# Optimization experiments

Hardware: AMD Instinct MI355X
Metric: run time of the kernel (lower is better)

## Reference

```python
import jax, jax.numpy as jnp
import numpy as np

NEG_MASK = -10000.0

def _sanitize(x):
    # torch.nan_to_num(x, nan=0.0, posinf=1.0, neginf=-1.0)
    return jnp.nan_to_num(x, nan=0.0, posinf=1.0, neginf=-1.0)

def setup_inputs() -> dict:
    key = jax.random.key(0)
    ks = jax.random.split(key, 7)
    Na, Nb, d = 4096, 4096, 256
    h = 4
    a_z = jax.random.normal(ks[0], (Na, d), dtype=jnp.float32)
    bv_z = jax.random.normal(ks[1], (Nb, d), dtype=jnp.float32)
    mask = jax.random.randint(ks[2], (Na, Nb), 0, 2) == 1
    weight = jax.random.normal(ks[3], (Na, Nb), dtype=jnp.float32)
    Wq = jax.random.normal(ks[4], (d, d), dtype=jnp.float32) * (1.0 / np.sqrt(d))
    Wk = jax.random.normal(ks[5], (d, d), dtype=jnp.float32) * (1.0 / np.sqrt(d))
    Wv = jax.random.normal(ks[6], (d, d), dtype=jnp.float32) * (1.0 / np.sqrt(d))
    return {"a_z": a_z, "bv_z": bv_z, "mask": mask, "weight": weight,
            "Wq": Wq, "Wk": Wk, "Wv": Wv, "h": h}

def reference(a_z, bv_z, mask, weight, Wq, Wk, Wv, h):
    d = a_z.shape[-1]
    dk = d // h
    # nan/inf sanitization (unconditional; identity on finite inputs, matching torch path)
    a_z = _sanitize(a_z)
    bv_z = _sanitize(bv_z)
    # projections; nn.Linear: x @ W.T. Reshape to [N, h, dk]
    q = (a_z @ Wq.T).reshape(-1, h, dk)   # [Na, h, dk]
    k = (bv_z @ Wk.T).reshape(-1, h, dk)  # [Nb, h, dk]
    v = (bv_z @ Wv.T).reshape(-1, h, dk)  # [Nb, h, dk]
    # attention scores [Na, h, Nb]
    att = jnp.einsum('ahd,bhd->ahb', q, k) / np.float32(np.sqrt(dk))
    att = jnp.where(mask[:, None, :], att, NEG_MASK)
    w = _sanitize(weight)
    att = att + w[:, None, :]
    att = jnp.clip(att, -10.0, 10.0)
    p = jax.nn.softmax(att, axis=-1)  # stable softmax (max-subtract) as in original
    # context: [Na, h, dk]; topic_align mean over heads -> [Na, dk]
    context = jnp.einsum('ahb,bhd->ahd', p, v)
    topic_align = context.mean(axis=1)
    influence = _sanitize(p.mean(axis=1).sum(axis=-1))  # [Na]
    return (topic_align, influence)
```

## Files before the change

### kernel.cpp

```cpp
#include <hip/hip_runtime.h>

#define NA 4096
#define NB 4096
#define DIM 256
#define DK 64
#define PSTR 72
#define WSTR 68
#define NSPLIT 8
#define BIT (NB / NSPLIT / 64)

typedef __attribute__((ext_vector_type(8))) short bf16x8;
typedef __attribute__((ext_vector_type(4))) float f32x4;
typedef __attribute__((ext_vector_type(4))) unsigned short us4;
typedef __attribute__((ext_vector_type(4))) int i32x4;

static __device__ __forceinline__ float bf2f(unsigned short u) {
    union { unsigned int u; float f; } x;
    x.u = ((unsigned int)u) << 16;
    return x.f;
}
static __device__ __forceinline__ unsigned short f2bf(float f) {
    union { float f; unsigned int u; } x;
    x.f = f;
    unsigned int r = x.u + 0x7fffu + ((x.u >> 16) & 1u);
    return (unsigned short)(r >> 16);
}


__global__ __launch_bounds__(256) void prep_kernel(
    const float* __restrict__ a_z, const float* __restrict__ bv,
    const float* __restrict__ Wq, const float* __restrict__ Wk,
    const float* __restrict__ Wv,
    unsigned short* __restrict__ ah, unsigned short* __restrict__ al,
    unsigned short* __restrict__ bh, unsigned short* __restrict__ bl,
    unsigned short* __restrict__ wh, unsigned short* __restrict__ wl)
{
    const int idx = blockIdx.x * 256 + threadIdx.x;
    const int y = blockIdx.y;
    const float* __restrict__ src;
    unsigned short* __restrict__ dh;
    unsigned short* __restrict__ dl;
    int row, col;
    if (y == 0) {
        src = a_z; dh = ah; dl = al;
        row = (idx >> 9) * 16 + (idx & 15);
        col = ((idx >> 6) & 7) * 32 + ((idx >> 4) & 3) * 8;
    } else if (y == 1) {
        src = bv; dh = bh; dl = bl;
        row = (idx >> 9) * 16 + (idx & 15);
        col = ((idx >> 6) & 7) * 32 + ((idx >> 4) & 3) * 8;
    } else {
        if (idx >= 3 * 8192) return;
        const int m = idx >> 13;
        const int im = idx & 8191;
        src = (m == 0) ? Wq : ((m == 1) ? Wk : Wv);
        dh = wh; dl = wl;
        row = (im >> 9) * 16 + (im & 15);
        col = ((im >> 6) & 7) * 32 + ((im >> 4) & 3) * 8;
    }
    f32x4 v0 = *(const f32x4*)(src + row * DIM + col);
    f32x4 v1 = *(const f32x4*)(src + row * DIM + col + 4);
    bf16x8 h8, l8;
    #pragma unroll
    for (int r = 0; r < 4; ++r) {
        unsigned short h0 = f2bf(v0[r]);
        h8[r] = (short)h0;  l8[r] = (short)f2bf(v0[r] - bf2f(h0));
        unsigned short h1 = f2bf(v1[r]);
        h8[4 + r] = (short)h1;  l8[4 + r] = (short)f2bf(v1[r] - bf2f(h1));
    }
    *(bf16x8*)(dh + idx * 8) = h8;
    *(bf16x8*)(dl + idx * 8) = l8;
}

__global__ __launch_bounds__(256, 2) void proj_kernel(
    const unsigned short* __restrict__ ah, const unsigned short* __restrict__ al,
    const unsigned short* __restrict__ bh, const unsigned short* __restrict__ bl,
    const unsigned short* __restrict__ whc, const unsigned short* __restrict__ wlc,
    unsigned short* __restrict__ qhi, unsigned short* __restrict__ qlo,
    unsigned short* __restrict__ khi, unsigned short* __restrict__ vtout)
{
    const int mat = blockIdx.z;
    const unsigned short* __restrict__ Xh = (mat == 0) ? ah : bh;
    const unsigned short* __restrict__ Xl = (mat == 0) ? al : bl;
    const unsigned short* __restrict__ Wh = whc + mat * 65536;
    const unsigned short* __restrict__ Wl = wlc + mat * 65536;

    const int tid  = threadIdx.x;
    const int wv   = tid >> 6;
    const int lane = tid & 63;
    const int c    = lane & 15;
    const int quad = lane >> 4;
    const int n0 = blockIdx.x * 64;
    const int by = blockIdx.y;

    const unsigned short* xhp = Xh + (n0 >> 4) * 4096 + lane * 8;
    const unsigned short* xlp = Xl + (n0 >> 4) * 4096 + lane * 8;
    const unsigned short* whp = Wh + (by * 4 + wv) * 4096 + lane * 8;
    const unsigned short* wlp = Wl + (by * 4 + wv) * 4096 + lane * 8;

    f32x4 acc[4];
    #pragma unroll
    for (int nt = 0; nt < 4; ++nt) acc[nt] = (f32x4){0.f, 0.f, 0.f, 0.f};

    bf16x8 wAh, wAl, xAh[4], xAl[4];
    bf16x8 wBh, wBl, xBh[4], xBl[4];

    wAh = *(const bf16x8*)(whp);
    wAl = *(const bf16x8*)(wlp);
    #pragma unroll
    for (int nt = 0; nt < 4; ++nt) {
        xAh[nt] = *(const bf16x8*)(xhp + nt * 4096);
        xAl[nt] = *(const bf16x8*)(xlp + nt * 4096);
    }

    #pragma unroll
    for (int kk = 0; kk < 8; kk += 2) {
        wBh = *(const bf16x8*)(whp + (kk + 1) * 512);
        wBl = *(const bf16x8*)(wlp + (kk + 1) * 512);
        #pragma unroll
        for (int nt = 0; nt < 4; ++nt) {
            xBh[nt] = *(const bf16x8*)(xhp + nt * 4096 + (kk + 1) * 512);
            xBl[nt] = *(const bf16x8*)(xlp + nt * 4096 + (kk + 1) * 512);
        }
        #pragma unroll
        for (int nt = 0; nt < 4; ++nt) {
            acc[nt] = __builtin_amdgcn_mfma_f32_16x16x32_bf16(xAh[nt], wAh, acc[nt], 0, 0, 0);
            acc[nt] = __builtin_amdgcn_mfma_f32_16x16x32_bf16(xAl[nt], wAh, acc[nt], 0, 0, 0);
            acc[nt] = __builtin_amdgcn_mfma_f32_16x16x32_bf16(xAh[nt], wAl, acc[nt], 0, 0, 0);
        }
        if (kk + 2 < 8) {
            wAh = *(const bf16x8*)(whp + (kk + 2) * 512);
            wAl = *(const bf16x8*)(wlp + (kk + 2) * 512);
            #pragma unroll
            for (int nt = 0; nt < 4; ++nt) {
                xAh[nt] = *(const bf16x8*)(xhp + nt * 4096 + (kk + 2) * 512);
                xAl[nt] = *(const bf16x8*)(xlp + nt * 4096 + (kk + 2) * 512);
            }
        }
        #pragma unroll
        for (int nt = 0; nt < 4; ++nt) {
            acc[nt] = __builtin_amdgcn_mfma_f32_16x16x32_bf16(xBh[nt], wBh, acc[nt], 0, 0, 0);
            acc[nt] = __builtin_amdgcn_mfma_f32_16x16x32_bf16(xBl[nt], wBh, acc[nt], 0, 0, 0);
            acc[nt] = __builtin_amdgcn_mfma_f32_16x16x32_bf16(xBh[nt], wBl, acc[nt], 0, 0, 0);
        }
    }

    if (mat != 2) {
        const int ks = wv >> 1;
        const int lq = ((wv & 1) * 2 + (c >> 3)) * 16 + quad * 4;
        const int e  = c & 7;
        #pragma unroll
        for (int nt = 0; nt < 4; ++nt) {
            const int tbase = (((by * 256 + (n0 >> 4) + nt) * 2 + ks) * 64 + lq) * 8 + e;
            #pragma unroll
            for (int r = 0; r < 4; ++r) {
                const int idx = tbase + r * 8;
                if (mat == 0) {
                    unsigned short h = f2bf(acc[nt][r]);
                    qhi[idx] = h;
                    qlo[idx] = f2bf(acc[nt][r] - bf2f(h));
                } else {
                    khi[idx] = f2bf(acc[nt][r]);
                }
            }
        }
    } else {
        #pragma unroll
        for (int nt = 0; nt < 4; ++nt) {
            const int lv = ((nt & 1) * 2 + (quad >> 1)) * 16 + c;
            const int idx = ((((by * 64 + (n0 >> 6)) * 4 + wv) * 2 + (nt >> 1)) * 64 + lv) * 8
                            + (quad & 1) * 4;
            us4 p;
            #pragma unroll
            for (int r = 0; r < 4; ++r) p[r] = f2bf(acc[nt][r]);
            *(us4*)(vtout + idx) = p;
        }
    }
}

__global__ __launch_bounds__(256, 2) void attn_kernel(
    const unsigned short* __restrict__ qhg,
    const unsigned short* __restrict__ qlg,
    const unsigned short* __restrict__ kg,
    const unsigned short* __restrict__ vtg,
    const float* __restrict__ wg,
    const int* __restrict__ mg,
    float* __restrict__ pnum,
    float* __restrict__ pden)
{
    __shared__ float wmbuf[2][16 * WSTR];
    __shared__ unsigned short pbuf[4][16 * PSTR];

    const int tid  = threadIdx.x;
    const int wv   = tid >> 6;
    const int lane = tid & 63;
    const int c    = lane & 15;
    const int quad = lane >> 4;

    const int flat = blockIdx.y * 256 + blockIdx.x;
    const int swz  = (flat & 7) * 256 + (flat >> 3);
    const int a0   = (swz & 255) * 16;
    const int bs   = swz >> 8;
    const int bbase = bs * (NB / NSPLIT);

    const int sa = tid >> 4;
    const int sb = (tid & 15) * 4;

    unsigned kbase = (unsigned)((wv * 256 + (bbase >> 4)) * 1024 + lane * 8);
    unsigned vbase = (unsigned)((wv * 64 + (bbase >> 6)) * 4096 + lane * 8);
    const unsigned qbase = (unsigned)((wv * 256 + (a0 >> 4)) * 1024 + lane * 8);

    bf16x8 qh[2], ql[2];
    qh[0] = *(const bf16x8*)(qhg + qbase);
    qh[1] = *(const bf16x8*)(qhg + qbase + 512);
    ql[0] = *(const bf16x8*)(qlg + qbase);
    ql[1] = *(const bf16x8*)(qlg + qbase + 512);

    bf16x8 ones;
    #pragma unroll
    for (int r = 0; r < 8; ++r) ones[r] = (short)0x3F80;

    f32x4 num[4];
    #pragma unroll
    for (int nt = 0; nt < 4; ++nt) num[nt] = (f32x4){0.f, 0.f, 0.f, 0.f};
    f32x4 dacc = (f32x4){0.f, 0.f, 0.f, 0.f};

    unsigned woff = (unsigned)((a0 + sa) * NB + bbase + sb);

    {
        f32x4 w = *(const f32x4*)(wg + woff);
        i32x4 m = *(const i32x4*)(mg + woff);
        f32x4 wm;
        #pragma unroll
        for (int r = 0; r < 4; ++r) wm[r] = m[r] ? w[r] : -1.0e9f;
        *(f32x4*)(&wmbuf[0][sa * WSTR + sb]) = wm;
    }
    woff += 64;

    for (int it = 0; it < BIT; ++it) {
        const int cur = it & 1;
        const bool more = (it + 1 < BIT);
        __syncthreads();

        bf16x8 kf[4][2];
        #pragma unroll
        for (int bt = 0; bt < 4; ++bt)
            #pragma unroll
            for (int ks = 0; ks < 2; ++ks)
                kf[bt][ks] = *(const bf16x8*)(kg + kbase + bt * 1024 + ks * 512);
        __builtin_amdgcn_sched_barrier(0);

        bf16x8 vf[4][2];
        #pragma unroll
        for (int nt = 0; nt < 4; ++nt)
            #pragma unroll
            for (int ks2 = 0; ks2 < 2; ++ks2)
                vf[nt][ks2] = *(const bf16x8*)(vtg + vbase + nt * 1024 + ks2 * 512);
        __builtin_amdgcn_sched_barrier(0);

        f32x4 wnxt; i32x4 mnxt;
        if (more) {
            wnxt = *(const f32x4*)(wg + woff);
            mnxt = *(const i32x4*)(mg + woff);
        }
        __builtin_amdgcn_sched_barrier(0);

        kbase += 4096;
        vbase += 4096;
        woff  += 64;

        f32x4 wf[4];
        #pragma unroll
        for (int bt = 0; bt < 4; ++bt)
            wf[bt] = *(const f32x4*)(&wmbuf[cur][c * WSTR + bt * 16 + quad * 4]);

        f32x4 S[4];
        __builtin_amdgcn_s_setprio(1);
        #pragma unroll
        for (int bt = 0; bt < 4; ++bt) {
            f32x4 s = (f32x4){0.f, 0.f, 0.f, 0.f};
            s = __builtin_amdgcn_mfma_f32_16x16x32_bf16(kf[bt][0], qh[0], s, 0, 0, 0);
            s = __builtin_amdgcn_mfma_f32_16x16x32_bf16(kf[bt][1], qh[1], s, 0, 0, 0);
            s = __builtin_amdgcn_mfma_f32_16x16x32_bf16(kf[bt][0], ql[0], s, 0, 0, 0);
            s = __builtin_amdgcn_mfma_f32_16x16x32_bf16(kf[bt][1], ql[1], s, 0, 0, 0);
            S[bt] = s;
        }
        __builtin_amdgcn_s_setprio(0);

        #pragma unroll
        for (int bt = 0; bt < 4; ++bt) {
            us4 p;
            #pragma unroll
            for (int r = 0; r < 4; ++r) {
                float t = fmaf(S[bt][r], 0.125f, wf[bt][r]);
                t = __builtin_amdgcn_fmed3f(t, -10.0f, 10.0f);
                float e = exp2f(t * 1.4426950408889634f);
                p[r] = f2bf(e);
            }
            *(us4*)(&pbuf[wv][c * PSTR + bt * 16 + quad * 4]) = p;
        }

        bf16x8 pf[2];
        #pragma unroll
        for (int ks2 = 0; ks2 < 2; ++ks2)
            pf[ks2] = *(const bf16x8*)(&pbuf[wv][c * PSTR + ks2 * 32 + quad * 8]);
        __builtin_amdgcn_s_setprio(1);
        #pragma unroll
        for (int nt = 0; nt < 4; ++nt) {
            num[nt] = __builtin_amdgcn_mfma_f32_16x16x32_bf16(pf[0], vf[nt][0], num[nt], 0, 0, 0);
            num[nt] = __builtin_amdgcn_mfma_f32_16x16x32_bf16(pf[1], vf[nt][1], num[nt], 0, 0, 0);
        }
        dacc = __builtin_amdgcn_mfma_f32_16x16x32_bf16(pf[0], ones, dacc, 0, 0, 0);
        dacc = __builtin_amdgcn_mfma_f32_16x16x32_bf16(pf[1], ones, dacc, 0, 0, 0);
        __builtin_amdgcn_s_setprio(0);

        if (more) {
            f32x4 wm;
            #pragma unroll
            for (int r = 0; r < 4; ++r) wm[r] = mnxt[r] ? wnxt[r] : -1.0e9f;
            *(f32x4*)(&wmbuf[cur ^ 1][sa * WSTR + sb]) = wm;
        }
    }

    const int hb = (bs * 4 + wv) * NA + a0;
    if (c == 0) {
        #pragma unroll
        for (int r = 0; r < 4; ++r)
            pden[hb + quad * 4 + r] = dacc[r];
    }

    #pragma unroll
    for (int nt = 0; nt < 4; ++nt)
        #pragma unroll
        for (int r = 0; r < 4; ++r)
            pnum[(size_t)(hb + quad * 4 + r) * DK + nt * 16 + c] = num[nt][r];
}

__global__ __launch_bounds__(256) void reduce_kernel(
    const float* __restrict__ pnum, const float* __restrict__ pden,
    float* __restrict__ outp)
{
    const int idx = blockIdx.x * 256 + threadIdx.x;
    const int a = idx >> 6, dd = idx & 63;
    float s = 0.0f;
    #pragma unroll
    for (int h = 0; h < 4; ++h) {
        float n = 0.0f, d = 0.0f;
        #pragma unroll
        for (int b = 0; b < NSPLIT; ++b) {
            n += pnum[(size_t)((b * 4 + h) * NA + a) * DK + dd];
            d += pden[(b * 4 + h) * NA + a];
        }
        s += n / d;
    }
    outp[idx] = 0.25f * s;
    if (dd == 0) outp[NA * DK + a] = 1.0f;
}

extern "C" void kernel_launch(void* const* d_in, const int* in_sizes, int n_in,
                              void* d_out, int out_size, void* d_ws, size_t ws_size,
                              hipStream_t stream) {
    const float* a_z = (const float*)d_in[0];
    const float* bv  = (const float*)d_in[1];
    const int* mask  = (const int*)d_in[2];
    const float* wgt = (const float*)d_in[3];
    const float* Wq  = (const float*)d_in[4];
    const float* Wk  = (const float*)d_in[5];
    const float* Wv  = (const float*)d_in[6];
    float* out = (float*)d_out;

    unsigned short* qhi = (unsigned short*)d_ws;
    unsigned short* qlo = qhi + NA * DIM;
    unsigned short* khi = qlo + NA * DIM;
    unsigned short* vt  = khi + NB * DIM;
    float* pnum = (float*)(vt + (size_t)DIM * NB);
    float* pden = pnum + (size_t)NSPLIT * 4 * NA * DK;
    unsigned short* ah  = (unsigned short*)pnum;
    unsigned short* al  = ah + NA * DIM;
    unsigned short* bh  = al + NA * DIM;
    unsigned short* bl  = bh + NB * DIM;
    unsigned short* whc = bl + NB * DIM;
    unsigned short* wlc = whc + 3 * 65536;

    prep_kernel<<<dim3(512, 3), 256, 0, stream>>>(a_z, bv, Wq, Wk, Wv,
                                                  ah, al, bh, bl, whc, wlc);
    proj_kernel<<<dim3(64, 4, 3), 256, 0, stream>>>(ah, al, bh, bl, whc, wlc,
                                                    qhi, qlo, khi, vt);
    attn_kernel<<<dim3(256, NSPLIT), 256, 0, stream>>>(qhi, qlo, khi, vt,
                                                       wgt, mask, pnum, pden);
    reduce_kernel<<<dim3(NA * DK / 256), 256, 0, stream>>>(pnum, pden, out);
}
```

Measured before the change: 215.8 us.

## Double-buffer K fragments across iterations and use packed bf16 conversion

Loads the K fragments for the next tile during the current tile's QK MFMAs, ping-ponging between two register sets via a macro-unrolled loop, so global K loads overlap compute instead of stalling at loop start. Replaces the manual bf16 rounding with the hardware v_cvt_pk_bf16_f32 packed convert instruction. The K double-buffering adds register pressure, which may reduce occupancy.

```diff
diff --git a/kernel.cpp b/kernel.cpp
--- a/kernel.cpp
+++ b/kernel.cpp
@@ -13,6 +13,7 @@
 typedef __attribute__((ext_vector_type(4))) float f32x4;
 typedef __attribute__((ext_vector_type(4))) unsigned short us4;
 typedef __attribute__((ext_vector_type(4))) int i32x4;
+typedef __attribute__((ext_vector_type(2))) unsigned int u32x2;
 
 static __device__ __forceinline__ float bf2f(unsigned short u) {
     union { unsigned int u; float f; } x;
@@ -237,90 +238,106 @@
     }
     woff += 64;
 
-    for (int it = 0; it < BIT; ++it) {
-        const int cur = it & 1;
-        const bool more = (it + 1 < BIT);
-        __syncthreads();
-
-        bf16x8 kf[4][2];
-        #pragma unroll
-        for (int bt = 0; bt < 4; ++bt)
-            #pragma unroll
-            for (int ks = 0; ks < 2; ++ks)
-                kf[bt][ks] = *(const bf16x8*)(kg + kbase + bt * 1024 + ks * 512);
-        __builtin_amdgcn_sched_barrier(0);
-
-        bf16x8 vf[4][2];
-        #pragma unroll
-        for (int nt = 0; nt < 4; ++nt)
-            #pragma unroll
-            for (int ks2 = 0; ks2 < 2; ++ks2)
-                vf[nt][ks2] = *(const bf16x8*)(vtg + vbase + nt * 1024 + ks2 * 512);
-        __builtin_amdgcn_sched_barrier(0);
-
-        f32x4 wnxt; i32x4 mnxt;
-        if (more) {
-            wnxt = *(const f32x4*)(wg + woff);
-            mnxt = *(const i32x4*)(mg + woff);
-        }
-        __builtin_amdgcn_sched_barrier(0);
-
-        kbase += 4096;
-        vbase += 4096;
-        woff  += 64;
-
-        f32x4 wf[4];
-        #pragma unroll
-        for (int bt = 0; bt < 4; ++bt)
-            wf[bt] = *(const f32x4*)(&wmbuf[cur][c * WSTR + bt * 16 + quad * 4]);
-
-        f32x4 S[4];
-        __builtin_amdgcn_s_setprio(1);
-        #pragma unroll
-        for (int bt = 0; bt < 4; ++bt) {
-            f32x4 s = (f32x4){0.f, 0.f, 0.f, 0.f};
-            s = __builtin_amdgcn_mfma_f32_16x16x32_bf16(kf[bt][0], qh[0], s, 0, 0, 0);
-            s = __builtin_amdgcn_mfma_f32_16x16x32_bf16(kf[bt][1], qh[1], s, 0, 0, 0);
-            s = __builtin_amdgcn_mfma_f32_16x16x32_bf16(kf[bt][0], ql[0], s, 0, 0, 0);
-            s = __builtin_amdgcn_mfma_f32_16x16x32_bf16(kf[bt][1], ql[1], s, 0, 0, 0);
-            S[bt] = s;
-        }
-        __builtin_amdgcn_s_setprio(0);
-
-        #pragma unroll
-        for (int bt = 0; bt < 4; ++bt) {
-            us4 p;
-            #pragma unroll
-            for (int r = 0; r < 4; ++r) {
-                float t = fmaf(S[bt][r], 0.125f, wf[bt][r]);
-                t = __builtin_amdgcn_fmed3f(t, -10.0f, 10.0f);
-                float e = exp2f(t * 1.4426950408889634f);
-                p[r] = f2bf(e);
-            }
-            *(us4*)(&pbuf[wv][c * PSTR + bt * 16 + quad * 4]) = p;
-        }
-
-        bf16x8 pf[2];
-        #pragma unroll
-        for (int ks2 = 0; ks2 < 2; ++ks2)
-            pf[ks2] = *(const bf16x8*)(&pbuf[wv][c * PSTR + ks2 * 32 + quad * 8]);
-        __builtin_amdgcn_s_setprio(1);
-        #pragma unroll
-        for (int nt = 0; nt < 4; ++nt) {
-            num[nt] = __builtin_amdgcn_mfma_f32_16x16x32_bf16(pf[0], vf[nt][0], num[nt], 0, 0, 0);
-            num[nt] = __builtin_amdgcn_mfma_f32_16x16x32_bf16(pf[1], vf[nt][1], num[nt], 0, 0, 0);
-        }
-        dacc = __builtin_amdgcn_mfma_f32_16x16x32_bf16(pf[0], ones, dacc, 0, 0, 0);
-        dacc = __builtin_amdgcn_mfma_f32_16x16x32_bf16(pf[1], ones, dacc, 0, 0, 0);
-        __builtin_amdgcn_s_setprio(0);
-
-        if (more) {
-            f32x4 wm;
-            #pragma unroll
-            for (int r = 0; r < 4; ++r) wm[r] = mnxt[r] ? wnxt[r] : -1.0e9f;
-            *(f32x4*)(&wmbuf[cur ^ 1][sa * WSTR + sb]) = wm;
-        }
-    }
+    bf16x8 kA[4][2], kB[4][2];
+    #pragma unroll
+    for (int bt = 0; bt < 4; ++bt)
+        #pragma unroll
+        for (int ks = 0; ks < 2; ++ks)
+            kA[bt][ks] = *(const bf16x8*)(kg + kbase + bt * 1024 + ks * 512);
+    kbase += 4096;
+
+#define ITER(IT, KCUR, KNXT)                                                   \
+    {                                                                          \
+        const int cur = (IT) & 1;                                              \
+        const bool more = ((IT) + 1 < BIT);                                    \
+        __syncthreads();              \
+                                      \
+        bf16x8 vf[4][2];                                                       \
+        _Pragma("unroll")                                                      \
+        for (int nt = 0; nt < 4; ++nt)                                         \
+            _Pragma("unroll")                                                  \
+            for (int ks2 = 0; ks2 < 2; ++ks2)                                  \
+                vf[nt][ks2] = *(const bf16x8*)(vtg + vbase + nt * 1024 + ks2 * 512); \
+                          \
+        f32x4 wnxt; i32x4 mnxt;                                                \
+        if (more) {                                                            \
+            wnxt = *(const f32x4*)(wg + woff);                                 \
+            mnxt = *(const i32x4*)(mg + woff);                                 \
+        }                                                                      \
+        __builtin_amdgcn_sched_barrier(0);                                     \
+                          \
+        f32x4 S[4];                                                            \
+        __builtin_amdgcn_s_setprio(1);                                         \
+        _Pragma("unroll")                                                      \
+        for (int bt = 0; bt < 4; ++bt) {                                       \
+            f32x4 s = (f32x4){0.f, 0.f, 0.f, 0.f};                             \
+            s = __builtin_amdgcn_mfma_f32_16x16x32_bf16(KCUR[bt][0], qh[0], s, 0, 0, 0); \
+            s = __builtin_amdgcn_mfma_f32_16x16x32_bf16(KCUR[bt][1], qh[1], s, 0, 0, 0); \
+            s = __builtin_amdgcn_mfma_f32_16x16x32_bf16(KCUR[bt][0], ql[0], s, 0, 0, 0); \
+            s = __builtin_amdgcn_mfma_f32_16x16x32_bf16(KCUR[bt][1], ql[1], s, 0, 0, 0); \
+            S[bt] = s;                                                         \
+        }                                                                      \
+        __builtin_amdgcn_s_setprio(0);                                         \
+                  \
+        if (more) {                                                            \
+            _Pragma("unroll")                                                  \
+            for (int bt = 0; bt < 4; ++bt)                                     \
+                _Pragma("unroll")                                              \
+                for (int ks = 0; ks < 2; ++ks)                                 \
+                    KNXT[bt][ks] = *(const bf16x8*)(kg + kbase + bt * 1024 + ks * 512); \
+        }                                                                      \
+        __builtin_amdgcn_sched_barrier(0);                                     \
+        kbase += 4096; vbase += 4096; woff += 64;                              \
+                                            \
+        f32x4 wf[4];                                                           \
+        _Pragma("unroll")                                                      \
+        for (int bt = 0; bt < 4; ++bt)                                         \
+            wf[bt] = *(const f32x4*)(&wmbuf[cur][c * WSTR + bt * 16 + quad * 4]); \
+        \
+        _Pragma("unroll")                                                      \
+        for (int bt = 0; bt < 4; ++bt) {                                       \
+            float ev[4];                                                       \
+            _Pragma("unroll")                                                  \
+            for (int r = 0; r < 4; ++r) {                                      \
+                float t = fmaf(S[bt][r], 0.125f, wf[bt][r]);                   \
+                t = __builtin_amdgcn_fmed3f(t, -10.0f, 10.0f);                 \
+                ev[r] = exp2f(t * 1.4426950408889634f);                        \
+            }                                                                  \
+            unsigned p0, p1;                                                   \
+            asm("v_cvt_pk_bf16_f32 %0, %1, %2" : "=v"(p0) : "v"(ev[0]), "v"(ev[1])); \
+            asm("v_cvt_pk_bf16_f32 %0, %1, %2" : "=v"(p1) : "v"(ev[2]), "v"(ev[3])); \
+            u32x2 pp; pp[0] = p0; pp[1] = p1;                                  \
+            *(u32x2*)(&pbuf[wv][c * PSTR + bt * 16 + quad * 4]) = pp;          \
+        }                                                                      \
+                            \
+        bf16x8 pf[2];                                                          \
+        _Pragma("unroll")                                                      \
+        for (int ks2 = 0; ks2 < 2; ++ks2)                                      \
+            pf[ks2] = *(const bf16x8*)(&pbuf[wv][c * PSTR + ks2 * 32 + quad * 8]); \
+        __builtin_amdgcn_s_setprio(1);                                         \
+        _Pragma("unroll")                                                      \
+        for (int nt = 0; nt < 4; ++nt) {                                       \
+            num[nt] = __builtin_amdgcn_mfma_f32_16x16x32_bf16(pf[0], vf[nt][0], num[nt], 0, 0, 0); \
+            num[nt] = __builtin_amdgcn_mfma_f32_16x16x32_bf16(pf[1], vf[nt][1], num[nt], 0, 0, 0); \
+        }                                                                      \
+        dacc = __builtin_amdgcn_mfma_f32_16x16x32_bf16(pf[0], ones, dacc, 0, 0, 0); \
+        dacc = __builtin_amdgcn_mfma_f32_16x16x32_bf16(pf[1], ones, dacc, 0, 0, 0); \
+        __builtin_amdgcn_s_setprio(0);                                         \
+               \
+        if (more) {                                                            \
+            f32x4 wm;                                                          \
+            _Pragma("unroll")                                                  \
+            for (int r = 0; r < 4; ++r) wm[r] = mnxt[r] ? wnxt[r] : -1.0e9f;   \
+            *(f32x4*)(&wmbuf[cur ^ 1][sa * WSTR + sb]) = wm;                   \
+        }                                                                      \
+    }
+
+    #pragma unroll
+    for (int ito = 0; ito < BIT; ito += 2) {
+        ITER(ito,     kA, kB)
+        ITER(ito + 1, kB, kA)
+    }
+#undef ITER
 
     const int hb = (bs * 4 + wv) * NA + a0;
     if (c == 0) {
```

New measurement: 232.3 us. 7.6% more time.

## Process two 16-row query tiles per block to reuse K/V fragments

Applied to the files above, without the earlier changes.

Each attention block now covers 32 query rows, two 16-row sub-tiles, instead of 16, so every K and V fragment loaded from global memory feeds twice as many MFMAs. The grid is halved and the weight/mask staging is widened to match. This cuts the K/V load traffic per query row. In exchange it raises register pressure from the doubled accumulators, score tiles and Q fragments, and leaves fewer blocks to fill the GPU.

```diff
diff --git a/kernel.cpp b/kernel.cpp
--- a/kernel.cpp
+++ b/kernel.cpp
@@ -188,8 +188,8 @@
     float* __restrict__ pnum,
     float* __restrict__ pden)
 {
-    __shared__ float wmbuf[2][16 * WSTR];
-    __shared__ unsigned short pbuf[4][16 * PSTR];
+    __shared__ float wmbuf[2][32 * WSTR];
+    __shared__ unsigned short pbuf[4][2][16 * PSTR];
 
     const int tid  = threadIdx.x;
     const int wv   = tid >> 6;
@@ -197,43 +197,56 @@
     const int c    = lane & 15;
     const int quad = lane >> 4;
 
-    const int flat = blockIdx.y * 256 + blockIdx.x;
-    const int swz  = (flat & 7) * 256 + (flat >> 3);
-    const int a0   = (swz & 255) * 16;
-    const int bs   = swz >> 8;
+    const int flat = blockIdx.y * 128 + blockIdx.x;
+    const int swz  = (flat & 7) * 128 + (flat >> 3);
+    const int a0   = (swz & 127) * 32;
+    const int bs   = swz >> 7;
     const int bbase = bs * (NB / NSPLIT);
 
-    const int sa = tid >> 4;
-    const int sb = (tid & 15) * 4;
+    const int sa = tid >> 3;
+    const int sb = (tid & 7) * 8;
 
     unsigned kbase = (unsigned)((wv * 256 + (bbase >> 4)) * 1024 + lane * 8);
     unsigned vbase = (unsigned)((wv * 64 + (bbase >> 6)) * 4096 + lane * 8);
     const unsigned qbase = (unsigned)((wv * 256 + (a0 >> 4)) * 1024 + lane * 8);
 
-    bf16x8 qh[2], ql[2];
-    qh[0] = *(const bf16x8*)(qhg + qbase);
-    qh[1] = *(const bf16x8*)(qhg + qbase + 512);
-    ql[0] = *(const bf16x8*)(qlg + qbase);
-    ql[1] = *(const bf16x8*)(qlg + qbase + 512);
+    bf16x8 qh[2][2], ql[2][2];
+    #pragma unroll
+    for (int at = 0; at < 2; ++at) {
+        qh[at][0] = *(const bf16x8*)(qhg + qbase + at * 1024);
+        qh[at][1] = *(const bf16x8*)(qhg + qbase + at * 1024 + 512);
+        ql[at][0] = *(const bf16x8*)(qlg + qbase + at * 1024);
+        ql[at][1] = *(const bf16x8*)(qlg + qbase + at * 1024 + 512);
+    }
 
     bf16x8 ones;
     #pragma unroll
     for (int r = 0; r < 8; ++r) ones[r] = (short)0x3F80;
 
-    f32x4 num[4];
-    #pragma unroll
-    for (int nt = 0; nt < 4; ++nt) num[nt] = (f32x4){0.f, 0.f, 0.f, 0.f};
-    f32x4 dacc = (f32x4){0.f, 0.f, 0.f, 0.f};
+    f32x4 num[2][4];
+    f32x4 dacc[2];
+    #pragma unroll
+    for (int at = 0; at < 2; ++at) {
+        #pragma unroll
+        for (int nt = 0; nt < 4; ++nt) num[at][nt] = (f32x4){0.f, 0.f, 0.f, 0.f};
+        dacc[at] = (f32x4){0.f, 0.f, 0.f, 0.f};
+    }
 
     unsigned woff = (unsigned)((a0 + sa) * NB + bbase + sb);
 
     {
-        f32x4 w = *(const f32x4*)(wg + woff);
-        i32x4 m = *(const i32x4*)(mg + woff);
-        f32x4 wm;
-        #pragma unroll
-        for (int r = 0; r < 4; ++r) wm[r] = m[r] ? w[r] : -1.0e9f;
-        *(f32x4*)(&wmbuf[0][sa * WSTR + sb]) = wm;
+        f32x4 w0 = *(const f32x4*)(wg + woff);
+        f32x4 w1 = *(const f32x4*)(wg + woff + 4);
+        i32x4 m0 = *(const i32x4*)(mg + woff);
+        i32x4 m1 = *(const i32x4*)(mg + woff + 4);
+        f32x4 wma, wmb;
+        #pragma unroll
+        for (int r = 0; r < 4; ++r) {
+            wma[r] = m0[r] ? w0[r] : -1.0e9f;
+            wmb[r] = m1[r] ? w1[r] : -1.0e9f;
+        }
+        *(f32x4*)(&wmbuf[0][sa * WSTR + sb])     = wma;
+        *(f32x4*)(&wmbuf[0][sa * WSTR + sb + 4]) = wmb;
     }
     woff += 64;
 
@@ -258,82 +271,92 @@
                 vf[nt][ks2] = *(const bf16x8*)(vtg + vbase + nt * 1024 + ks2 * 512);
         __builtin_amdgcn_sched_barrier(0);
 
-        f32x4 wnxt; i32x4 mnxt;
+        f32x4 wn0, wn1; i32x4 mn0, mn1;
         if (more) {
-            wnxt = *(const f32x4*)(wg + woff);
-            mnxt = *(const i32x4*)(mg + woff);
+            wn0 = *(const f32x4*)(wg + woff);
+            wn1 = *(const f32x4*)(wg + woff + 4);
+            mn0 = *(const i32x4*)(mg + woff);
+            mn1 = *(const i32x4*)(mg + woff + 4);
         }
         __builtin_amdgcn_sched_barrier(0);
 
-        kbase += 4096;
-        vbase += 4096;
-        woff  += 64;
-
-        f32x4 wf[4];
-        #pragma unroll
-        for (int bt = 0; bt < 4; ++bt)
-            wf[bt] = *(const f32x4*)(&wmbuf[cur][c * WSTR + bt * 16 + quad * 4]);
-
-        f32x4 S[4];
+        kbase += 4096; vbase += 4096; woff += 64;
+
+        f32x4 S[2][4];
         __builtin_amdgcn_s_setprio(1);
         #pragma unroll
-        for (int bt = 0; bt < 4; ++bt) {
-            f32x4 s = (f32x4){0.f, 0.f, 0.f, 0.f};
-            s = __builtin_amdgcn_mfma_f32_16x16x32_bf16(kf[bt][0], qh[0], s, 0, 0, 0);
-            s = __builtin_amdgcn_mfma_f32_16x16x32_bf16(kf[bt][1], qh[1], s, 0, 0, 0);
-            s = __builtin_amdgcn_mfma_f32_16x16x32_bf16(kf[bt][0], ql[0], s, 0, 0, 0);
-            s = __builtin_amdgcn_mfma_f32_16x16x32_bf16(kf[bt][1], ql[1], s, 0, 0, 0);
-            S[bt] = s;
-        }
+        for (int at = 0; at < 2; ++at)
+            #pragma unroll
+            for (int bt = 0; bt < 4; ++bt) {
+                f32x4 s = (f32x4){0.f, 0.f, 0.f, 0.f};
+                s = __builtin_amdgcn_mfma_f32_16x16x32_bf16(kf[bt][0], qh[at][0], s, 0, 0, 0);
+                s = __builtin_amdgcn_mfma_f32_16x16x32_bf16(kf[bt][1], qh[at][1], s, 0, 0, 0);
+                s = __builtin_amdgcn_mfma_f32_16x16x32_bf16(kf[bt][0], ql[at][0], s, 0, 0, 0);
+                s = __builtin_amdgcn_mfma_f32_16x16x32_bf16(kf[bt][1], ql[at][1], s, 0, 0, 0);
+                S[at][bt] = s;
+            }
         __builtin_amdgcn_s_setprio(0);
 
         #pragma unroll
-        for (int bt = 0; bt < 4; ++bt) {
-            us4 p;
+        for (int at = 0; at < 2; ++at) {
+            #pragma unroll
+            for (int bt = 0; bt < 4; ++bt) {
+                f32x4 wf = *(const f32x4*)(&wmbuf[cur][(at * 16 + c) * WSTR + bt * 16 + quad * 4]);
+                us4 p;
+                #pragma unroll
+                for (int r = 0; r < 4; ++r) {
+                    float t = fmaf(S[at][bt][r], 0.125f, wf[r]);
+                    t = __builtin_amdgcn_fmed3f(t, -10.0f, 10.0f);
+                    float e = exp2f(t * 1.4426950408889634f);
+                    p[r] = f2bf(e);
+                }
+                *(us4*)(&pbuf[wv][at][c * PSTR + bt * 16 + quad * 4]) = p;
+            }
+        }
+
+        __builtin_amdgcn_s_setprio(1);
+        #pragma unroll
+        for (int at = 0; at < 2; ++at) {
+            bf16x8 pf[2];
+            #pragma unroll
+            for (int ks2 = 0; ks2 < 2; ++ks2)
+                pf[ks2] = *(const bf16x8*)(&pbuf[wv][at][c * PSTR + ks2 * 32 + quad * 8]);
+            #pragma unroll
+            for (int nt = 0; nt < 4; ++nt) {
+                num[at][nt] = __builtin_amdgcn_mfma_f32_16x16x32_bf16(pf[0], vf[nt][0], num[at][nt], 0, 0, 0);
+                num[at][nt] = __builtin_amdgcn_mfma_f32_16x16x32_bf16(pf[1], vf[nt][1], num[at][nt], 0, 0, 0);
+            }
+            dacc[at] = __builtin_amdgcn_mfma_f32_16x16x32_bf16(pf[0], ones, dacc[at], 0, 0, 0);
+            dacc[at] = __builtin_amdgcn_mfma_f32_16x16x32_bf16(pf[1], ones, dacc[at], 0, 0, 0);
+        }
+        __builtin_amdgcn_s_setprio(0);
+
+        if (more) {
+            f32x4 wma, wmb;
             #pragma unroll
             for (int r = 0; r < 4; ++r) {
-                float t = fmaf(S[bt][r], 0.125f, wf[bt][r]);
-                t = __builtin_amdgcn_fmed3f(t, -10.0f, 10.0f);
-                float e = exp2f(t * 1.4426950408889634f);
-                p[r] = f2bf(e);
-            }
-            *(us4*)(&pbuf[wv][c * PSTR + bt * 16 + quad * 4]) = p;
-        }
-
-        bf16x8 pf[2];
-        #pragma unroll
-        for (int ks2 = 0; ks2 < 2; ++ks2)
-            pf[ks2] = *(const bf16x8*)(&pbuf[wv][c * PSTR + ks2 * 32 + quad * 8]);
-        __builtin_amdgcn_s_setprio(1);
-        #pragma unroll
-        for (int nt = 0; nt < 4; ++nt) {
-            num[nt] = __builtin_amdgcn_mfma_f32_16x16x32_bf16(pf[0], vf[nt][0], num[nt], 0, 0, 0);
-            num[nt] = __builtin_amdgcn_mfma_f32_16x16x32_bf16(pf[1], vf[nt][1], num[nt], 0, 0, 0);
-        }
-        dacc = __builtin_amdgcn_mfma_f32_16x16x32_bf16(pf[0], ones, dacc, 0, 0, 0);
-        dacc = __builtin_amdgcn_mfma_f32_16x16x32_bf16(pf[1], ones, dacc, 0, 0, 0);
-        __builtin_amdgcn_s_setprio(0);
-
-        if (more) {
-            f32x4 wm;
-            #pragma unroll
-            for (int r = 0; r < 4; ++r) wm[r] = mnxt[r] ? wnxt[r] : -1.0e9f;
-            *(f32x4*)(&wmbuf[cur ^ 1][sa * WSTR + sb]) = wm;
-        }
-    }
-
-    const int hb = (bs * 4 + wv) * NA + a0;
-    if (c == 0) {
-        #pragma unroll
-        for (int r = 0; r < 4; ++r)
-            pden[hb + quad * 4 + r] = dacc[r];
-    }
-
-    #pragma unroll
-    for (int nt = 0; nt < 4; ++nt)
-        #pragma unroll
-        for (int r = 0; r < 4; ++r)
-            pnum[(size_t)(hb + quad * 4 + r) * DK + nt * 16 + c] = num[nt][r];
+                wma[r] = mn0[r] ? wn0[r] : -1.0e9f;
+                wmb[r] = mn1[r] ? wn1[r] : -1.0e9f;
+            }
+            *(f32x4*)(&wmbuf[cur ^ 1][sa * WSTR + sb])     = wma;
+            *(f32x4*)(&wmbuf[cur ^ 1][sa * WSTR + sb + 4]) = wmb;
+        }
+    }
+
+    #pragma unroll
+    for (int at = 0; at < 2; ++at) {
+        const int hb = (bs * 4 + wv) * NA + a0 + at * 16;
+        if (c == 0) {
+            #pragma unroll
+            for (int r = 0; r < 4; ++r)
+                pden[hb + quad * 4 + r] = dacc[at][r];
+        }
+        #pragma unroll
+        for (int nt = 0; nt < 4; ++nt)
+            #pragma unroll
+            for (int r = 0; r < 4; ++r)
+                pnum[(size_t)(hb + quad * 4 + r) * DK + nt * 16 + c] = num[at][nt][r];
+    }
 }
 
 __global__ __launch_bounds__(256) void reduce_kernel(
@@ -386,7 +409,7 @@
                                                   ah, al, bh, bl, whc, wlc);
     proj_kernel<<<dim3(64, 4, 3), 256, 0, stream>>>(ah, al, bh, bl, whc, wlc,
                                                     qhi, qlo, khi, vt);
-    attn_kernel<<<dim3(256, NSPLIT), 256, 0, stream>>>(qhi, qlo, khi, vt,
+    attn_kernel<<<dim3(128, NSPLIT), 256, 0, stream>>>(qhi, qlo, khi, vt,
                                                        wgt, mask, pnum, pden);
     reduce_kernel<<<dim3(NA * DK / 256), 256, 0, stream>>>(pnum, pden, out);
 }
```

Result: faster. 207.9 us (-3.7%).
